# Optimization experiments

Measured on AMD Instinct MI355X. Metric: run time of the kernel, lower is better.

The kernel has to match this reference:

```python
import jax, jax.numpy as jnp
import numpy as np

EPS = 1e-9
# ((top,bottom),(left,right)) zero-pads for the 8 neighbor directions,
# matching torch nn.ZeroPad2d((l,r,t,b)) order gate1..gate8 in the source.
PADS = [((0, 2), (0, 2)), ((0, 2), (1, 1)), ((0, 2), (2, 0)),
        ((1, 1), (0, 2)), ((1, 1), (2, 0)),
        ((2, 0), (0, 2)), ((2, 0), (1, 1)), ((2, 0), (2, 0))]


def _pad8(x):
    # x: (B,H,W) -> (B,8,H+2,W+2): 8 directional zero-padded shifts
    return jnp.stack([jnp.pad(x, ((0, 0), tb, lr)) for tb, lr in PADS], axis=1)


def _affinity_normalization(guidance):
    # guidance: (B,8,H,W) -> gate_wb (B,8,H+2,W+2), gate_sum (B,H,W)
    gate_wb = jnp.stack(
        [jnp.pad(guidance[:, k], ((0, 0), tb, lr)) for k, (tb, lr) in enumerate(PADS)],
        axis=1)
    abs_weight = jnp.sum(jnp.abs(gate_wb), axis=1, keepdims=True)
    gate_wb = gate_wb / (abs_weight + EPS)
    gate_sum = jnp.sum(gate_wb, axis=1)[:, 1:-1, 1:-1]
    return gate_wb, gate_sum


def setup_inputs() -> dict:
    key = jax.random.key(0)
    k1, k2, k3, k4 = jax.random.split(key, 4)
    B, H, W = 2, 384, 1280
    guidance = jax.random.normal(k1, (B, 8, H, W), dtype=jnp.float32)
    blur_depth = jax.random.uniform(k2, (B, 1, H, W), dtype=jnp.float32) * 80.0
    valid = (jax.random.uniform(k3, (B, 1, H, W)) < 0.05).astype(jnp.float32)
    sparse_depth = valid * jax.random.uniform(k4, (B, 1, H, W), dtype=jnp.float32) * 80.0
    return {"guidance": guidance, "blur_depth": blur_depth,
            "sparse_depth": sparse_depth, "prop_time": 24}


def reference(guidance, blur_depth, sparse_depth, prop_time):
    # CSPN affinity-guided iterative propagation (norm_type='8sum')
    gate_wb, gate_sum = _affinity_normalization(guidance)
    raw = blur_depth[:, 0]                       # (B,H,W)
    sparse_mask = jnp.sign(sparse_depth[:, 0])   # (B,H,W), 1 where valid
    d = raw
    for _ in range(prop_time):
        # weighted sum over 8 padded neighbor shifts, then crop halo
        nws = jnp.sum(gate_wb * _pad8(d), axis=1)[:, 1:-1, 1:-1]
        d = (1.0 - gate_sum) * raw + nws
        d = (1.0 - sparse_mask) * d + sparse_mask * raw
    return d  # (B,H,W), matches result_depth.squeeze(1)
```

## Files before the change

kernel.cpp:

```cpp
#include <hip/hip_runtime.h>
#include <hip/hip_fp16.h>

static constexpr int Hh = 384;
static constexpr int Ww = 1280;
static constexpr int HW = Hh * Ww;
static constexpr int NPIX = 2 * HW;
static constexpr int TILE = 32;
static constexpr int S = 6;
static constexpr int R = TILE + 2 * S;
static constexpr int RR = R * R;
static constexpr int BLOCK = 256;
static constexpr int PPQ = (RR + BLOCK - 1) / BLOCK;
static constexpr int TI = Hh / TILE;
static constexpr int TJ = Ww / TILE;
static constexpr int GRID = 2 * TI * TJ;
static constexpr int T = 24;
static constexpr float EPSF = 1e-9f;

__device__ __constant__ int DI_c[8] = { 1, 1, 1, 0, 0, -1, -1, -1 };
__device__ __constant__ int DJ_c[8] = { 1, 0, -1, 1, -1, 1, 0, -1 };

__global__ void affinity_norm(const float* __restrict__ g,
                              const float* __restrict__ raw,
                              const float* __restrict__ sparse,
                              __half* __restrict__ wbuf,
                              float* __restrict__ cbuf) {
    int idx = blockIdx.x * blockDim.x + threadIdx.x;
    if (idx >= NPIX) return;
    int b = idx / HW;
    int r = idx - b * HW;
    int i = r / Ww;
    int j = r - i * Ww;

    const float* gb = g + (size_t)b * 8 * HW;
    float v[8];
    float a = EPSF;
#pragma unroll
    for (int k = 0; k < 8; k++) {
        int ii = i + DI_c[k], jj = j + DJ_c[k];
        float gv = 0.0f;
        if (ii >= 0 && ii < Hh && jj >= 0 && jj < Ww)
            gv = gb[k * HW + ii * Ww + jj];
        v[k] = gv;
        a += fabsf(gv);
    }
    float inv = 1.0f / a, gs = 0.0f;
#pragma unroll
    for (int k = 0; k < 8; k++) { v[k] *= inv; gs += v[k]; }

    float rawv = raw[idx];
    bool m = sparse[idx] > 0.0f;
    cbuf[idx] = m ? rawv : (1.0f - gs) * rawv;
    __half wv[8];
#pragma unroll
    for (int k = 0; k < 8; k++) wv[k] = __float2half(m ? 0.0f : v[k]);
    *(float4*)(wbuf + (size_t)idx * 8) = *(const float4*)wv;
}

__global__ __launch_bounds__(BLOCK, 4) void fused_steps(
    const __half* __restrict__ wbuf, const float* __restrict__ cbuf,
    const float* __restrict__ din, float* __restrict__ dout)
{
    __shared__ float sd[2][RR];

    const int tid = threadIdx.x;
    int bx = blockIdx.x;
    const int tj = bx % TJ; bx /= TJ;
    const int ti = bx % TI;
    const int b  = bx / TI;
    const int oi = ti * TILE - S;
    const int oj = tj * TILE - S;

    float4 wv[PPQ];
    float  C[PPQ];
    unsigned edgemask = 0;

#pragma unroll
    for (int q = 0; q < PPQ; q++) {
        int p = tid + q * BLOCK;
        if (p < RR) {
            int ri = p / R, rj = p - ri * R;
            int gi = oi + ri, gj = oj + rj;
            int gic = min(max(gi, 0), Hh - 1);
            int gjc = min(max(gj, 0), Ww - 1);
            int idx = b * HW + gic * Ww + gjc;
            sd[0][p] = din[idx];
            wv[q] = *(const float4*)(wbuf + (size_t)idx * 8);
            C[q]  = cbuf[idx];
            if (ri == 0 || ri == R - 1 || rj == 0 || rj == R - 1)
                edgemask |= 1u << q;
        }
    }
    __syncthreads();

    int cur = 0;
    for (int s = 1; s < S; s++) {
        const float* s0 = sd[cur];
        float* s1 = sd[cur ^ 1];
#pragma unroll
        for (int q = 0; q < PPQ; q++) {
            int p = tid + q * BLOCK;
            if (p >= RR) continue;
            float v;
            if ((edgemask >> q) & 1) {
                v = s0[p];
            } else {
                const __half2* wh = (const __half2*)&wv[q];
                float2 w01 = __half22float2(wh[0]);
                float2 w23 = __half22float2(wh[1]);
                float2 w45 = __half22float2(wh[2]);
                float2 w67 = __half22float2(wh[3]);
                v = w01.x * s0[p + R + 1] + w01.y * s0[p + R] + w23.x * s0[p + R - 1]
                  + w23.y * s0[p + 1]     + w45.x * s0[p - 1]
                  + w45.y * s0[p - R + 1] + w67.x * s0[p - R] + w67.y * s0[p - R - 1]
                  + C[q];
            }
            s1[p] = v;
        }
        __syncthreads();
        cur ^= 1;
    }

    const float* s0 = sd[cur];
#pragma unroll
    for (int q = 0; q < PPQ; q++) {
        int p = tid + q * BLOCK;
        if (p >= RR) continue;
        int ri = p / R, rj = p - ri * R;
        if (ri >= S && ri < R - S && rj >= S && rj < R - S) {
            const __half2* wh = (const __half2*)&wv[q];
            float2 w01 = __half22float2(wh[0]);
            float2 w23 = __half22float2(wh[1]);
            float2 w45 = __half22float2(wh[2]);
            float2 w67 = __half22float2(wh[3]);
            float v = w01.x * s0[p + R + 1] + w01.y * s0[p + R] + w23.x * s0[p + R - 1]
                    + w23.y * s0[p + 1]     + w45.x * s0[p - 1]
                    + w45.y * s0[p - R + 1] + w67.x * s0[p - R] + w67.y * s0[p - R - 1]
                    + C[q];
            int gi = oi + ri, gj = oj + rj;
            dout[b * HW + gi * Ww + gj] = v;
        }
    }
}

extern "C" void kernel_launch(void* const* d_in, const int* in_sizes, int n_in,
                              void* d_out, int out_size, void* d_ws, size_t ws_size,
                              hipStream_t stream) {
    const float* guidance = (const float*)d_in[0];
    const float* blur     = (const float*)d_in[1];
    const float* sparse   = (const float*)d_in[2];
    float* out = (float*)d_out;

    char* ws = (char*)d_ws;
    float* bufA = (float*)ws;
    float* bufB = bufA + NPIX;
    __half* wbuf = (__half*)(bufB + NPIX);
    float*  cbuf = (float*)(wbuf + (size_t)NPIX * 8);

    const int threads = 256;
    const int blocks = (NPIX + threads - 1) / threads;
    affinity_norm<<<blocks, threads, 0, stream>>>(guidance, blur, sparse, wbuf, cbuf);

    fused_steps<<<GRID, BLOCK, 0, stream>>>(wbuf, cbuf, blur, bufA);
    fused_steps<<<GRID, BLOCK, 0, stream>>>(wbuf, cbuf, bufA, bufB);
    fused_steps<<<GRID, BLOCK, 0, stream>>>(wbuf, cbuf, bufB, bufA);
    fused_steps<<<GRID, BLOCK, 0, stream>>>(wbuf, cbuf, bufA, out);
}
```

Measured before the change: 151.7 us.

## Shrink stencil steps to valid cone, pre-convert weights, remap blocks across XCDs

Each step now updates only interior pixels whose distance to the region border is at least the current step, so the invalid halo cone is no longer computed. Border cells are copied into both shared buffers once instead of on every step. Weights are converted from half to float once at load time and kept in registers, which removes repeated conversions but raises register pressure and may lower occupancy. Block indices are remapped so that neighbouring tiles land on the same XCD, which is meant to improve L2 reuse of overlapping halos.

```diff
diff --git a/kernel.cpp b/kernel.cpp
--- a/kernel.cpp
+++ b/kernel.cpp
@@ -9,12 +9,16 @@
 static constexpr int S = 6;
 static constexpr int R = TILE + 2 * S;
 static constexpr int RR = R * R;
+static constexpr int ISIDE = R - 2;
+static constexpr int NINT = ISIDE * ISIDE;
 static constexpr int BLOCK = 256;
 static constexpr int PPQ = (RR + BLOCK - 1) / BLOCK;
+static constexpr int PPI = (NINT + BLOCK - 1) / BLOCK;
 static constexpr int TI = Hh / TILE;
 static constexpr int TJ = Ww / TILE;
 static constexpr int GRID = 2 * TI * TJ;
-static constexpr int T = 24;
+static constexpr int NXCD = 8;
+static constexpr int CHUNK = GRID / NXCD;
 static constexpr float EPSF = 1e-9f;
 
 __device__ __constant__ int DI_c[8] = { 1, 1, 1, 0, 0, -1, -1, -1 };
@@ -64,58 +68,75 @@
     __shared__ float sd[2][RR];
 
     const int tid = threadIdx.x;
-    int bx = blockIdx.x;
+    int bx = (blockIdx.x % NXCD) * CHUNK + blockIdx.x / NXCD;
     const int tj = bx % TJ; bx /= TJ;
     const int ti = bx % TI;
     const int b  = bx / TI;
     const int oi = ti * TILE - S;
     const int oj = tj * TILE - S;
 
-    float4 wv[PPQ];
-    float  C[PPQ];
-    unsigned edgemask = 0;
-
 #pragma unroll
     for (int q = 0; q < PPQ; q++) {
         int p = tid + q * BLOCK;
         if (p < RR) {
             int ri = p / R, rj = p - ri * R;
-            int gi = oi + ri, gj = oj + rj;
-            int gic = min(max(gi, 0), Hh - 1);
-            int gjc = min(max(gj, 0), Ww - 1);
+            int gic = min(max(oi + ri, 0), Hh - 1);
+            int gjc = min(max(oj + rj, 0), Ww - 1);
+            float v = din[b * HW + gic * Ww + gjc];
+            sd[0][p] = v;
+            if (ri == 0 || ri == R - 1 || rj == 0 || rj == R - 1)
+                sd[1][p] = v;
+        }
+    }
+
+    float w[PPI][8];
+    float C[PPI];
+    int   pp[PPI];
+    int   rng[PPI];
+#pragma unroll
+    for (int q = 0; q < PPI; q++) {
+        int pi = tid + q * BLOCK;
+        if (pi < NINT) {
+            int r0 = pi / ISIDE;
+            int ri = 1 + r0, rj = 1 + (pi - r0 * ISIDE);
+            int p = ri * R + rj;
+            pp[q]  = p;
+            rng[q] = min(min(ri, R - 1 - ri), min(rj, R - 1 - rj));
+            int gic = min(max(oi + ri, 0), Hh - 1);
+            int gjc = min(max(oj + rj, 0), Ww - 1);
             int idx = b * HW + gic * Ww + gjc;
-            sd[0][p] = din[idx];
-            wv[q] = *(const float4*)(wbuf + (size_t)idx * 8);
-            C[q]  = cbuf[idx];
-            if (ri == 0 || ri == R - 1 || rj == 0 || rj == R - 1)
-                edgemask |= 1u << q;
+            float4 wv = *(const float4*)(wbuf + (size_t)idx * 8);
+            const __half2* wh = (const __half2*)&wv;
+            float2 w01 = __half22float2(wh[0]);
+            float2 w23 = __half22float2(wh[1]);
+            float2 w45 = __half22float2(wh[2]);
+            float2 w67 = __half22float2(wh[3]);
+            w[q][0] = w01.x; w[q][1] = w01.y; w[q][2] = w23.x; w[q][3] = w23.y;
+            w[q][4] = w45.x; w[q][5] = w45.y; w[q][6] = w67.x; w[q][7] = w67.y;
+            C[q] = cbuf[idx];
+        } else {
+            rng[q] = 0;
+            pp[q] = 0;
         }
     }
     __syncthreads();
 
     int cur = 0;
+#pragma unroll
     for (int s = 1; s < S; s++) {
         const float* s0 = sd[cur];
         float* s1 = sd[cur ^ 1];
 #pragma unroll
-        for (int q = 0; q < PPQ; q++) {
-            int p = tid + q * BLOCK;
-            if (p >= RR) continue;
-            float v;
-            if ((edgemask >> q) & 1) {
-                v = s0[p];
-            } else {
-                const __half2* wh = (const __half2*)&wv[q];
-                float2 w01 = __half22float2(wh[0]);
-                float2 w23 = __half22float2(wh[1]);
-                float2 w45 = __half22float2(wh[2]);
-                float2 w67 = __half22float2(wh[3]);
-                v = w01.x * s0[p + R + 1] + w01.y * s0[p + R] + w23.x * s0[p + R - 1]
-                  + w23.y * s0[p + 1]     + w45.x * s0[p - 1]
-                  + w45.y * s0[p - R + 1] + w67.x * s0[p - R] + w67.y * s0[p - R - 1]
-                  + C[q];
+        for (int q = 0; q < PPI; q++) {
+            if (rng[q] >= s) {
+                int p = pp[q];
+                float v = C[q]
+                    + w[q][0] * s0[p + R + 1] + w[q][1] * s0[p + R]
+                    + w[q][2] * s0[p + R - 1] + w[q][3] * s0[p + 1]
+                    + w[q][4] * s0[p - 1]     + w[q][5] * s0[p - R + 1]
+                    + w[q][6] * s0[p - R]     + w[q][7] * s0[p - R - 1];
+                s1[p] = v;
             }
-            s1[p] = v;
         }
         __syncthreads();
         cur ^= 1;
@@ -123,22 +144,16 @@
 
     const float* s0 = sd[cur];
 #pragma unroll
-    for (int q = 0; q < PPQ; q++) {
-        int p = tid + q * BLOCK;
-        if (p >= RR) continue;
-        int ri = p / R, rj = p - ri * R;
-        if (ri >= S && ri < R - S && rj >= S && rj < R - S) {
-            const __half2* wh = (const __half2*)&wv[q];
-            float2 w01 = __half22float2(wh[0]);
-            float2 w23 = __half22float2(wh[1]);
-            float2 w45 = __half22float2(wh[2]);
-            float2 w67 = __half22float2(wh[3]);
-            float v = w01.x * s0[p + R + 1] + w01.y * s0[p + R] + w23.x * s0[p + R - 1]
-                    + w23.y * s0[p + 1]     + w45.x * s0[p - 1]
-                    + w45.y * s0[p - R + 1] + w67.x * s0[p - R] + w67.y * s0[p - R - 1]
-                    + C[q];
-            int gi = oi + ri, gj = oj + rj;
-            dout[b * HW + gi * Ww + gj] = v;
+    for (int q = 0; q < PPI; q++) {
+        if (rng[q] >= S) {
+            int p = pp[q];
+            float v = C[q]
+                + w[q][0] * s0[p + R + 1] + w[q][1] * s0[p + R]
+                + w[q][2] * s0[p + R - 1] + w[q][3] * s0[p + 1]
+                + w[q][4] * s0[p - 1]     + w[q][5] * s0[p - R + 1]
+                + w[q][6] * s0[p - R]     + w[q][7] * s0[p - R - 1];
+            int ri = p / R, rj = p - ri * R;
+            dout[b * HW + (oi + ri) * Ww + (oj + rj)] = v;
         }
     }
 }
```

After: 142.5 us. 1.06x faster.
